# Optimization experiments

Measured on AMD Instinct MI355X. Metric: run time of the kernel, lower is better.

Reference implementation:

```python
import jax, jax.numpy as jnp
import numpy as np

B, N, DIM = 64, 784, 256
N1, N2, HS, WS, M, D = 1, 4, 28, 7, 8, 2  # x_windows, y_windows, H_sp, W_sp, num_heads, d
HW = HS * WS                              # 196 tokens per window
C = DIM // M                              # 32 channels per head


def setup_inputs() -> dict:
    key = jax.random.key(0)
    ks = jax.random.split(key, 5)
    x = jax.random.normal(ks[0], (B, N, DIM), dtype=jnp.float32)
    Wc = jax.random.normal(ks[1], (DIM, M * D), dtype=jnp.float32) * 0.02
    bc = jax.random.normal(ks[2], (M * D,), dtype=jnp.float32) * 0.02
    Wg = jax.random.normal(ks[3], (HW * D, HW * HW), dtype=jnp.float32) * 0.02
    bg = jax.random.normal(ks[4], (HW * HW,), dtype=jnp.float32) * 0.02
    return {"x": x, "Wc": Wc, "bc": bc, "Wg": Wg, "bg": bg}


def reference(x, Wc, bc, Wg, bg):
    b = x.shape[0]
    # compress: B N C -> B N (m d)
    w = x @ Wc + bc
    # rearrange 'b (n1 h n2 w) (m d) -> b (n1 n2 m) (h w d)'
    w = w.reshape(b, N1, HS, N2, WS, M, D)
    w = w.transpose(0, 1, 3, 5, 2, 4, 6).reshape(b, N1 * N2 * M, HW * D)
    # generate per-window mixing weights: B Nw (HW*HW)
    w = w @ Wg + bg
    w = w.reshape(b, N1 * N2 * M, HW, HW)
    # softmax over dim=-2 (the (h1 w1) source axis)
    w = jax.nn.softmax(w, axis=-2)
    # rearrange x: 'b (n1 h1 n2 w1) (m c) -> b (n1 n2 m) c (h1 w1)'
    xv = x.reshape(b, N1, HS, N2, WS, M, C)
    xv = xv.transpose(0, 1, 3, 5, 6, 2, 4).reshape(b, N1 * N2 * M, C, HW)
    # windowed mixing matmul: (b, Nw, C, HW) @ (b, Nw, HW, HW)
    out = jnp.matmul(xv, w)
    # rearrange back: 'b (n1 n2 m) c (h2 w2) -> b (n1 h2 n2 w2) (m c)'
    out = out.reshape(b, N1, N2, M, C, HS, WS)
    out = out.transpose(0, 1, 5, 2, 6, 3, 4).reshape(b, N1 * HS * N2 * WS, M * C)
    return out
```

## Files before the change

### kernel.cpp

```cpp
#include <hip/hip_runtime.h>
#include <hip/hip_bf16.h>
#include <stdint.h>
#include <stddef.h>

#define NB    64
#define NTOK  784
#define DIMC  256
#define NN2   4
#define NM    8
#define NHW   196
#define NWIN  32
#define NROWS 2048
#define NK    392
#define NKP   448
#define NBIG  38416
#define NIP   200
#define STROW 39200
#define STROW2 39232
#define NPT   39424
#define NTT   154
#define PTS   232

typedef __attribute__((ext_vector_type(4))) float f32x4;
typedef __attribute__((ext_vector_type(8))) short bf16x8;

static __device__ __forceinline__ float bf2f(unsigned short u) {
  union { unsigned int i; float f; } v; v.i = ((unsigned int)u) << 16; return v.f;
}
static __device__ __forceinline__ unsigned short f2bf(float f) {
  union { float f; unsigned int i; } v; v.f = f;
  unsigned int r = v.i + 0x7fffu + ((v.i >> 16) & 1u);
  return (unsigned short)(r >> 16);
}

__global__ __launch_bounds__(256) void k_compress(
    const float* __restrict__ x, const float* __restrict__ Wc,
    const float* __restrict__ bc, unsigned short* __restrict__ Abf) {
  __shared__ float wcs[16 * 256];
  __shared__ float bcs[16];
  const int tid = threadIdx.x;
  const int b  = blockIdx.x / NN2;
  const int n2 = blockIdx.x % NN2;
  for (int idx = tid; idx < 4096; idx += 256) {
    int c = idx >> 4, md = idx & 15;
    wcs[md * 256 + c] = Wc[idx];
  }
  if (tid < 16) bcs[tid] = bc[tid];
  __syncthreads();
  if (tid < NHW) {
    const int h = tid / 7, wcol = tid % 7;
    const int t = h * 28 + n2 * 7 + wcol;
    const float* xp = x + ((size_t)b * NTOK + t) * DIMC;
    float acc[16];
    #pragma unroll
    for (int md = 0; md < 16; ++md) acc[md] = bcs[md];
    for (int c = 0; c < 256; c += 4) {
      const f32x4 xv = *(const f32x4*)(xp + c);
      #pragma unroll
      for (int md = 0; md < 16; ++md) {
        const f32x4 wv = *(const f32x4*)(wcs + md * 256 + c);
        acc[md] += xv[0]*wv[0] + xv[1]*wv[1] + xv[2]*wv[2] + xv[3]*wv[3];
      }
    }
    #pragma unroll
    for (int md = 0; md < 16; ++md) {
      const int m = md >> 1, d = md & 1;
      const int r = b * NWIN + n2 * NM + m;
      Abf[(size_t)r * NKP + tid * 2 + d] = f2bf(acc[md]);
    }
  }
  for (int e = tid; e < NM * (NKP - NK); e += 256) {
    const int m = e / (NKP - NK);
    const int k = NK + (e % (NKP - NK));
    const int r = b * NWIN + n2 * NM + m;
    Abf[(size_t)r * NKP + k] = (k == NK) ? (unsigned short)0x3F80 : 0;
  }
}

__global__ __launch_bounds__(256) void k_wgt(
    const float* __restrict__ Wg, const float* __restrict__ bg,
    unsigned short* __restrict__ Wgbt) {
  __shared__ float tile[64][65];
  const int bid = blockIdx.x;
  const int n0 = (bid % 601) * 64;
  const int k0 = (bid / 601) * 64;
  const int tid = threadIdx.x;
  for (int idx = tid; idx < 4096; idx += 256) {
    const int kk = idx >> 6, nn = idx & 63;
    const int k = k0 + kk, n = n0 + nn;
    float v = 0.f;
    if (n < NBIG) {
      if (k < NK) v = Wg[(size_t)k * NBIG + n];
      else if (k == NK) v = bg[n];
    }
    tile[nn][kk] = v;
  }
  __syncthreads();
  for (int idx = tid; idx < 512; idx += 256) {
    const int nn = idx >> 3, gg = idx & 7;
    const int n = n0 + nn;
    if (n < NBIG) {
      const int i = n / NHW, j = n - (n / NHW) * NHW;
      const int np = j * NIP + i;
      unsigned short u8[8];
      #pragma unroll
      for (int e = 0; e < 8; ++e) u8[e] = f2bf(tile[nn][gg * 8 + e]);
      *(uint4*)&Wgbt[(size_t)np * NKP + k0 + gg * 8] = *(const uint4*)u8;
    }
  }
}

__global__ __launch_bounds__(256) void k_zero(unsigned short* __restrict__ Wgbt) {
  const int bid = blockIdx.x;
  int np;
  if (bid < 784) { const int j = bid >> 2, i = 196 + (bid & 3); np = j * NIP + i; }
  else           { np = STROW + (bid - 784); }
  unsigned int* p = (unsigned int*)(Wgbt + (size_t)np * NKP);
  if (threadIdx.x < 224) p[threadIdx.x] = 0u;
}

__global__ __launch_bounds__(512, 2) void k_gemm(
    const unsigned short* __restrict__ A,
    const unsigned short* __restrict__ Bt,
    unsigned short* __restrict__ E, int mtiles) {
  __shared__ __align__(128) short smem[65536];
  const int tid = threadIdx.x;
  const int w = tid >> 6, lane = tid & 63;
  const int nwg = gridDim.x;
  const int q = nwg >> 3, rr = nwg & 7;
  const int xcd = blockIdx.x & 7, pos = blockIdx.x >> 3;
  const int wg = (xcd < rr ? xcd * (q + 1) : rr * (q + 1) + (xcd - rr) * q) + pos;
  const int nt = wg / mtiles, mt = wg % mtiles;
  const int m0 = mt * 256, n0 = nt * 256;
  const int lrow = lane >> 3, lgran = lane & 7;
  const int srcg = (lgran ^ lrow) * 8;

  const unsigned short* srow = (w < 4)
      ? A  + (size_t)(m0 + w * 64 + lrow) * NKP + srcg
      : Bt + (size_t)(n0 + (w - 4) * 64 + lrow) * NKP + srcg;
  const int dstb0 = ((w < 4) ? 0 : 32768) + (w & 3) * 8192;

  auto stage = [&](int kt, int buf) {
    #pragma unroll
    for (int is = 0; is < 8; ++is) {
      __builtin_amdgcn_global_load_lds(
          (const __attribute__((address_space(1))) void*)(srow + (size_t)is * 8 * NKP + kt),
          (__attribute__((address_space(3))) void*)((char*)smem + buf * 65536 + dstb0 + is * 1024),
          16, 0, 0);
    }
  };

  const int wm0 = (w >> 1) * 64;
  const int wn0 = (w & 1) * 128;
  const int lq = lane >> 4, lx = lane & 7, cr = lane & 15;
  f32x4 acc[4][8] = {};

  stage(0, 0);
  #pragma unroll
  for (int t = 0; t < 7; ++t) {
    if (t < 6) {
      stage((t + 1) * 64, (t + 1) & 1);
      asm volatile("s_waitcnt vmcnt(8)" ::: "memory");
    } else {
      asm volatile("s_waitcnt vmcnt(0)" ::: "memory");
    }
    __builtin_amdgcn_s_barrier();
    asm volatile("" ::: "memory");
    const short* ab = smem + (t & 1) * 32768;
    const short* bb = ab + 16384;
    #pragma unroll
    for (int kk = 0; kk < 2; ++kk) {
      const int slot = ((kk * 4 + lq) ^ lx) * 8;
      bf16x8 af[4], bfr[8];
      #pragma unroll
      for (int mi = 0; mi < 4; ++mi)
        af[mi] = *(const bf16x8*)(ab + (wm0 + mi * 16 + cr) * 64 + slot);
      #pragma unroll
      for (int ni = 0; ni < 8; ++ni)
        bfr[ni] = *(const bf16x8*)(bb + (wn0 + ni * 16 + cr) * 64 + slot);
      #pragma unroll
      for (int mi = 0; mi < 4; ++mi)
        #pragma unroll
        for (int ni = 0; ni < 8; ++ni)
          acc[mi][ni] = __builtin_amdgcn_mfma_f32_16x16x32_bf16(af[mi], bfr[ni], acc[mi][ni], 0, 0, 0);
    }
    asm volatile("" ::: "memory");
    __builtin_amdgcn_s_barrier();
  }

  #pragma unroll
  for (int h = 0; h < 2; ++h) {
    if (h) {
      asm volatile("" ::: "memory");
      __builtin_amdgcn_s_barrier();
      asm volatile("" ::: "memory");
    }
    if ((w >> 2) == h) {
      #pragma unroll
      for (int mi = 0; mi < 4; ++mi)
        #pragma unroll
        for (int ni = 0; ni < 8; ++ni)
          #pragma unroll
          for (int e = 0; e < 4; ++e) {
            const int rl = wm0 - h * 128 + mi * 16 + lq * 4 + e;
            const int cl = wn0 + ni * 16 + cr;
            smem[rl * 264 + cl] = (short)f2bf(__expf(acc[mi][ni][e]));
          }
    }
    asm volatile("" ::: "memory");
    __builtin_amdgcn_s_barrier();
    asm volatile("" ::: "memory");
    for (int g = tid; g < 4096; g += 512) {
      const int rl = g >> 5, seg = g & 31;
      const int col0 = n0 + seg * 8;
      if (col0 < STROW2) {
        const uint4 v = *(const uint4*)&smem[rl * 264 + seg * 8];
        *(uint4*)&E[(size_t)(m0 + h * 128 + rl) * STROW2 + col0] = v;
      }
    }
  }
}

__global__ __launch_bounds__(512) void k_mix(
    const unsigned short* __restrict__ E, const float* __restrict__ x,
    float* __restrict__ out, int row0) {
  __shared__ unsigned short Elds[22528];
  __shared__ unsigned short xvT[32 * PTS];
  const int tid = threadIdx.x, w = tid >> 6, lane = tid & 63;
  const int row = blockIdx.x >> 1, jh = blockIdx.x & 1;
  const int r = row0 + row;
  const int b = r >> 5, win = r & 31, n2 = win >> 3, m = win & 7;

  const unsigned short* Eb = E + (size_t)row * STROW2;
  const int g0 = jh ? 2800 : 0;
  const int nch = jh ? 33 : 44;
  for (int ch = w; ch < nch; ch += 8) {
    const int gr = g0 + ch * 64 + lane;
    if (gr < 4904)
      __builtin_amdgcn_global_load_lds(
          (const __attribute__((address_space(1))) void*)(Eb + (size_t)gr * 8),
          (__attribute__((address_space(3))) void*)((char*)Elds + ch * 1024), 16, 0, 0);
  }

  for (int idx = tid; idx < 1568; idx += 512) {
    const int i = idx >> 3, c4 = (idx & 7) * 4;
    const int t = (i / 7) * 28 + n2 * 7 + (i % 7);
    const f32x4 v = *(const f32x4*)(x + ((size_t)b * NTOK + t) * DIMC + m * 32 + c4);
    xvT[(c4 + 0) * PTS + i] = f2bf(v[0]);
    xvT[(c4 + 1) * PTS + i] = f2bf(v[1]);
    xvT[(c4 + 2) * PTS + i] = f2bf(v[2]);
    xvT[(c4 + 3) * PTS + i] = f2bf(v[3]);
  }
  for (int idx = tid; idx < 32 * (PTS - NHW); idx += 512) {
    const int c = idx / (PTS - NHW), i = NHW + idx % (PTS - NHW);
    xvT[c * PTS + i] = 0;
  }
  __syncthreads();

  bf16x8 bfr[2][7];
  #pragma unroll
  for (int ct = 0; ct < 2; ++ct)
    #pragma unroll
    for (int kk = 0; kk < 7; ++kk)
      bfr[ct][kk] = *(const bf16x8*)&xvT[(ct * 16 + (lane & 15)) * PTS + kk * 32 + (lane >> 4) * 8];
  const bool den = (lane & 15) == 0;
  bf16x8 oneA, oneB;
  #pragma unroll
  for (int e = 0; e < 8; ++e) {
    oneA[e] = den ? (short)0x3F80 : (short)0;
    const int i6 = 192 + (lane >> 4) * 8 + e;
    oneB[e] = (den && i6 < NHW) ? (short)0x3F80 : (short)0;
  }

  const int jt0 = jh ? 7 : 0;
  const int jtend = jh ? 13 : 7;
  for (int jt = jt0 + w; jt < jtend; jt += 8) {
    const int jA = jt * 16 + (lane & 15);
    const int jAc = (jA < NHW) ? jA : NHW - 1;
    const unsigned short* rp = Elds + jAc * NIP - jh * 22400 + (lane >> 4) * 8;
    bf16x8 af[7];
    #pragma unroll
    for (int kk = 0; kk < 7; ++kk) af[kk] = *(const bf16x8*)(rp + kk * 32);
    f32x4 a0 = {0.f,0.f,0.f,0.f}, a1 = {0.f,0.f,0.f,0.f}, ad = {0.f,0.f,0.f,0.f};
    #pragma unroll
    for (int kk = 0; kk < 7; ++kk) {
      a0 = __builtin_amdgcn_mfma_f32_16x16x32_bf16(af[kk], bfr[0][kk], a0, 0, 0, 0);
      a1 = __builtin_amdgcn_mfma_f32_16x16x32_bf16(af[kk], bfr[1][kk], a1, 0, 0, 0);
      ad = __builtin_amdgcn_mfma_f32_16x16x32_bf16(af[kk], (kk < 6) ? oneA : oneB, ad, 0, 0, 0);
    }
    const int c = lane & 15;
    #pragma unroll
    for (int e = 0; e < 4; ++e) {
      const int j = jt * 16 + (lane >> 4) * 4 + e;
      const float dv = __shfl(ad[e], lane & 48);
      if (j < NHW) {
        const float inv = 1.f / dv;
        const int t2 = (j / 7) * 28 + n2 * 7 + (j % 7);
        float* op = out + ((size_t)b * NTOK + t2) * DIMC + m * 32;
        op[c] = a0[e] * inv;
        op[c + 16] = a1[e] * inv;
      }
    }
  }
}

extern "C" void kernel_launch(void* const* d_in, const int* in_sizes, int n_in,
                              void* d_out, int out_size, void* d_ws, size_t ws_size,
                              hipStream_t stream) {
  const float* x  = (const float*)d_in[0];
  const float* Wc = (const float*)d_in[1];
  const float* bc = (const float*)d_in[2];
  const float* Wg = (const float*)d_in[3];
  const float* bg = (const float*)d_in[4];
  float* out = (float*)d_out;

  char* ws = (char*)d_ws;
  const size_t wgbt_bytes = (size_t)NPT * NKP * 2;
  const size_t a_bytes    = (size_t)NROWS * NKP * 2;
  unsigned short* Wgbt = (unsigned short*)ws;
  unsigned short* Abf  = (unsigned short*)(ws + wgbt_bytes);
  unsigned short* E    = (unsigned short*)(ws + wgbt_bytes + a_bytes);
  const size_t fixed = wgbt_bytes + a_bytes;
  const size_t srow_bytes = (size_t)STROW2 * 2;

  size_t avail = (ws_size > fixed) ? (ws_size - fixed) : 0;
  int rows_chunk = (int)(avail / srow_bytes);
  rows_chunk = (rows_chunk / 256) * 256;
  if (rows_chunk > NROWS) rows_chunk = NROWS;
  if (rows_chunk < 256)  rows_chunk = 256;

  hipLaunchKernelGGL(k_compress, dim3(NB * NN2), dim3(256), 0, stream, x, Wc, bc, Abf);
  hipLaunchKernelGGL(k_wgt, dim3(601 * 7), dim3(256), 0, stream, Wg, bg, Wgbt);
  hipLaunchKernelGGL(k_zero, dim3(1008), dim3(256), 0, stream, Wgbt);
  for (int row0 = 0; row0 < NROWS; row0 += rows_chunk) {
    int rc = NROWS - row0; if (rc > rows_chunk) rc = rows_chunk;
    hipLaunchKernelGGL(k_gemm, dim3((rc / 256) * NTT), dim3(512), 0, stream,
                       Abf + (size_t)row0 * NKP, Wgbt, E, rc / 256);
    hipLaunchKernelGGL(k_mix, dim3(rc * 2), dim3(512), 0, stream, E, x, out, row0);
  }
}
```

Before: 221.5 us.

## Restructure GEMM main loop into four-phase interleaved load/MFMA schedule

Reworks the k_gemm inner loop. Warps are now laid out 2x4 (128x64 per warp instead of 64x128), and the global-to-LDS staging of the next k-tile is split into four phases, each issued between LDS fragment reads and an MFMA cluster. Around each MFMA cluster it adds sched_barrier and setprio, aiming to overlap memory traffic with matrix math across waves. The cost is many more barriers per k-step and a full vmcnt(0) drain before each buffer switch, which could add sync overhead.

```diff
diff --git a/kernel.cpp b/kernel.cpp
--- a/kernel.cpp
+++ b/kernel.cpp
@@ -18,7 +18,7 @@
 #define STROW 39200
 #define STROW2 39232
 #define NPT   39424
-#define NTT   154
+#define NTT2  154
 #define PTS   232
 
 typedef __attribute__((ext_vector_type(4))) float f32x4;
@@ -132,84 +132,90 @@
   const int wg = (xcd < rr ? xcd * (q + 1) : rr * (q + 1) + (xcd - rr) * q) + pos;
   const int nt = wg / mtiles, mt = wg % mtiles;
   const int m0 = mt * 256, n0 = nt * 256;
-  const int lrow = lane >> 3, lgran = lane & 7;
-  const int srcg = (lgran ^ lrow) * 8;
-
-  const unsigned short* srow = (w < 4)
-      ? A  + (size_t)(m0 + w * 64 + lrow) * NKP + srcg
-      : Bt + (size_t)(n0 + (w - 4) * 64 + lrow) * NKP + srcg;
-  const int dstb0 = ((w < 4) ? 0 : 32768) + (w & 3) * 8192;
-
-  auto stage = [&](int kt, int buf) {
-    #pragma unroll
-    for (int is = 0; is < 8; ++is) {
+  const int wr = w >> 2, wc = w & 3;
+  const int lrow = lane >> 3;
+  const int lcolsw = ((lane & 7) ^ lrow) * 8;
+
+  const unsigned short* Asrc = A  + (size_t)(m0 + w * 16 + lrow) * NKP + lcolsw;
+  const unsigned short* Bsrc = Bt + (size_t)(n0 + w * 16 + lrow) * NKP + lcolsw;
+
+  auto stageHalf = [&](const unsigned short* src, int opofs, int h, int buf, int kt) {
+    #pragma unroll
+    for (int is = 0; is < 2; ++is) {
       __builtin_amdgcn_global_load_lds(
-          (const __attribute__((address_space(1))) void*)(srow + (size_t)is * 8 * NKP + kt),
-          (__attribute__((address_space(3))) void*)((char*)smem + buf * 65536 + dstb0 + is * 1024),
+          (const __attribute__((address_space(1))) void*)(src + (size_t)(h * 128 + is * 8) * NKP + kt),
+          (__attribute__((address_space(3))) void*)((char*)smem + buf * 65536 + opofs + h * 16384 + (w * 2 + is) * 1024),
           16, 0, 0);
     }
   };
-
-  const int wm0 = (w >> 1) * 64;
-  const int wn0 = (w & 1) * 128;
+  auto stagePhase = [&](int ph, int jn) {
+    const int buf = jn & 1, kt = jn * 64;
+    if      (ph == 0) stageHalf(Asrc, 0,     0, buf, kt);
+    else if (ph == 1) stageHalf(Asrc, 0,     1, buf, kt);
+    else if (ph == 2) stageHalf(Bsrc, 32768, 0, buf, kt);
+    else              stageHalf(Bsrc, 32768, 1, buf, kt);
+  };
+
+  f32x4 acc[8][4] = {};
+  stagePhase(0, 0); stagePhase(1, 0); stagePhase(2, 0); stagePhase(3, 0);
+  asm volatile("s_waitcnt vmcnt(0)" ::: "memory");
+  __builtin_amdgcn_s_barrier();
+
   const int lq = lane >> 4, lx = lane & 7, cr = lane & 15;
-  f32x4 acc[4][8] = {};
-
-  stage(0, 0);
-  #pragma unroll
-  for (int t = 0; t < 7; ++t) {
-    if (t < 6) {
-      stage((t + 1) * 64, (t + 1) & 1);
-      asm volatile("s_waitcnt vmcnt(8)" ::: "memory");
-    } else {
+  bf16x8 af[4], bfr[4];
+  for (int j = 0; j < 7; ++j) {
+    const int buf = j & 1;
+    const short* ab = smem + buf * 32768;
+    const short* bb = ab + 16384;
+    const int arow0 = wr * 128, bcol0 = wc * 64;
+    #pragma unroll
+    for (int ph = 0; ph < 4; ++ph) {
+      const int kk = ph >> 1, mih = ph & 1;
+      const int slot = ((kk * 4 + lq) ^ lx) * 8;
+      #pragma unroll
+      for (int i = 0; i < 4; ++i)
+        af[i] = *(const bf16x8*)(ab + (arow0 + (mih * 4 + i) * 16 + cr) * 64 + slot);
+      if (mih == 0) {
+        #pragma unroll
+        for (int ni = 0; ni < 4; ++ni)
+          bfr[ni] = *(const bf16x8*)(bb + (bcol0 + ni * 16 + cr) * 64 + slot);
+      }
+      if (j < 6) stagePhase(ph, j + 1);
+      __builtin_amdgcn_s_barrier();
+      asm volatile("s_waitcnt lgkmcnt(0)" ::: "memory");
+      __builtin_amdgcn_sched_barrier(0);
+      __builtin_amdgcn_s_setprio(1);
+      #pragma unroll
+      for (int i = 0; i < 4; ++i)
+        #pragma unroll
+        for (int ni = 0; ni < 4; ++ni)
+          acc[mih * 4 + i][ni] = __builtin_amdgcn_mfma_f32_16x16x32_bf16(
+              af[i], bfr[ni], acc[mih * 4 + i][ni], 0, 0, 0);
+      __builtin_amdgcn_s_setprio(0);
+      __builtin_amdgcn_sched_barrier(0);
+      __builtin_amdgcn_s_barrier();
+    }
+    if (j < 6) {
       asm volatile("s_waitcnt vmcnt(0)" ::: "memory");
-    }
-    __builtin_amdgcn_s_barrier();
-    asm volatile("" ::: "memory");
-    const short* ab = smem + (t & 1) * 32768;
-    const short* bb = ab + 16384;
-    #pragma unroll
-    for (int kk = 0; kk < 2; ++kk) {
-      const int slot = ((kk * 4 + lq) ^ lx) * 8;
-      bf16x8 af[4], bfr[8];
-      #pragma unroll
-      for (int mi = 0; mi < 4; ++mi)
-        af[mi] = *(const bf16x8*)(ab + (wm0 + mi * 16 + cr) * 64 + slot);
-      #pragma unroll
-      for (int ni = 0; ni < 8; ++ni)
-        bfr[ni] = *(const bf16x8*)(bb + (wn0 + ni * 16 + cr) * 64 + slot);
-      #pragma unroll
-      for (int mi = 0; mi < 4; ++mi)
+      __builtin_amdgcn_s_barrier();
+    }
+  }
+
+  for (int h = 0; h < 2; ++h) {
+    if (h) __syncthreads();
+    if (wr == h) {
+      #pragma unroll
+      for (int mi = 0; mi < 8; ++mi)
         #pragma unroll
-        for (int ni = 0; ni < 8; ++ni)
-          acc[mi][ni] = __builtin_amdgcn_mfma_f32_16x16x32_bf16(af[mi], bfr[ni], acc[mi][ni], 0, 0, 0);
-    }
-    asm volatile("" ::: "memory");
-    __builtin_amdgcn_s_barrier();
-  }
-
-  #pragma unroll
-  for (int h = 0; h < 2; ++h) {
-    if (h) {
-      asm volatile("" ::: "memory");
-      __builtin_amdgcn_s_barrier();
-      asm volatile("" ::: "memory");
-    }
-    if ((w >> 2) == h) {
-      #pragma unroll
-      for (int mi = 0; mi < 4; ++mi)
-        #pragma unroll
-        for (int ni = 0; ni < 8; ++ni)
+        for (int ni = 0; ni < 4; ++ni)
           #pragma unroll
           for (int e = 0; e < 4; ++e) {
-            const int rl = wm0 - h * 128 + mi * 16 + lq * 4 + e;
-            const int cl = wn0 + ni * 16 + cr;
+            const int rl = mi * 16 + lq * 4 + e;
+            const int cl = wc * 64 + ni * 16 + cr;
             smem[rl * 264 + cl] = (short)f2bf(__expf(acc[mi][ni][e]));
           }
     }
-    asm volatile("" ::: "memory");
-    __builtin_amdgcn_s_barrier();
-    asm volatile("" ::: "memory");
+    __syncthreads();
     for (int g = tid; g < 4096; g += 512) {
       const int rl = g >> 5, seg = g & 31;
       const int col0 = n0 + seg * 8;
@@ -334,7 +340,7 @@
   hipLaunchKernelGGL(k_zero, dim3(1008), dim3(256), 0, stream, Wgbt);
   for (int row0 = 0; row0 < NROWS; row0 += rows_chunk) {
     int rc = NROWS - row0; if (rc > rows_chunk) rc = rows_chunk;
-    hipLaunchKernelGGL(k_gemm, dim3((rc / 256) * NTT), dim3(512), 0, stream,
+    hipLaunchKernelGGL(k_gemm, dim3((rc / 256) * NTT2), dim3(512), 0, stream,
                        Abf + (size_t)row0 * NKP, Wgbt, E, rc / 256);
     hipLaunchKernelGGL(k_mix, dim3(rc * 2), dim3(512), 0, stream, E, x, out, row0);
   }
```

Result: no change. 222.1 us (+0.3%).
